# Optimization experiments

Measured on AMD Instinct MI355X. Metric: run time of the kernel, lower is better.

Reference implementation:

```python
import jax, jax.numpy as jnp
import numpy as np

B, T, F, H, OUT = 32, 2048, 64, 256, 64
EPS = 1e-3  # Keras LayerNormalization default epsilon


def _gru(x_seq, kernel, rkernel, bias, return_sequences):
    """Keras GRU (reset_after=True). x_seq: [B,T,Fin]; kernel [Fin,3H]; rkernel [H,3H]; bias [2,3H]."""
    h = x_seq.shape[-1]
    Hd = rkernel.shape[0]
    # precompute input projections for all timesteps (one big GEMM)
    xb = jnp.einsum('btf,fg->btg', x_seq, kernel) + bias[0]  # [B,T,3H]

    def step(h_prev, xt):
        inner = h_prev @ rkernel + bias[1]            # [B,3H]
        xz, xr, xh = jnp.split(xt, 3, axis=-1)
        rz, rr, rh = jnp.split(inner, 3, axis=-1)
        z = jax.nn.sigmoid(xz + rz)
        r = jax.nn.sigmoid(xr + rr)
        hh = jnp.tanh(xh + r * rh)
        h_new = z * h_prev + (1.0 - z) * hh
        return h_new, h_new

    h0 = jnp.zeros((x_seq.shape[0], Hd), dtype=x_seq.dtype)
    h_last, seq = jax.lax.scan(step, h0, jnp.swapaxes(xb, 0, 1))  # scan over T
    if return_sequences:
        return jnp.swapaxes(seq, 0, 1)  # [B,T,H]
    return h_last  # [B,H]


def setup_inputs() -> dict:
    key = jax.random.key(0)
    ks = jax.random.split(key, 10)
    s = 0.05
    return {
        'x': jax.random.normal(ks[0], (B, T, F), dtype=jnp.float32),
        'gamma': jnp.ones((F,), jnp.float32),
        'beta': jnp.zeros((F,), jnp.float32),
        'k1': jax.random.normal(ks[1], (F, 3 * H), jnp.float32) * s,
        'rk1': jax.random.normal(ks[2], (H, 3 * H), jnp.float32) * s,
        'b1': jnp.zeros((2, 3 * H), jnp.float32),
        'k2': jax.random.normal(ks[3], (H, 3 * H), jnp.float32) * s,
        'rk2': jax.random.normal(ks[4], (H, 3 * H), jnp.float32) * s,
        'b2': jnp.zeros((2, 3 * H), jnp.float32),
        'wd': jax.random.normal(ks[5], (H, OUT), jnp.float32) * s,
        'bd': jnp.zeros((OUT,), jnp.float32),
    }


def reference(x, gamma, beta, k1, rk1, b1, k2, rk2, b2, wd, bd):
    # LayerNorm over last (feature) axis
    mu = jnp.mean(x, axis=-1, keepdims=True)
    var = jnp.mean(jnp.square(x - mu), axis=-1, keepdims=True)
    xn = (x - mu) * jax.lax.rsqrt(var + EPS) * gamma + beta
    h1 = _gru(xn, k1, rk1, b1, return_sequences=True)   # [B,T,H]
    h2 = _gru(h1, k2, rk2, b2, return_sequences=False)  # [B,H]
    return h2 @ wd + bd  # [B,OUT]
```

## Files before the change

kernel.cpp:

```cpp
#include <hip/hip_runtime.h>

#define B_    32
#define T_    2048
#define F_    64
#define H_    256
#define OUT_  64
#define G3_   768
#define NWG1  16
#define NWG2  16
#define TOTAL_WG (NWG1 + NWG2)
#define WGT   512

#define PBLK   512
#define XN_BYTES (B_ * T_ * F_ * 2)
#define S1_OFF   XN_BYTES
#define S2_OFF   (S1_OFF + 4 * 16 * PBLK * 2)
#define FLAG_OFF (S2_OFF + 2 * 16 * PBLK * 2)
#define PROG_OFF (FLAG_OFF + 2048)

typedef _Float16 half8 __attribute__((ext_vector_type(8)));
typedef _Float16 half4 __attribute__((ext_vector_type(4)));
typedef float    f32x4 __attribute__((ext_vector_type(4)));
typedef unsigned long long u64;

#define LD_A(p)    __hip_atomic_load((p),  __ATOMIC_RELAXED, __HIP_MEMORY_SCOPE_AGENT)
#define ST_A(p, v) __hip_atomic_store((p), (v), __ATOMIC_RELAXED, __HIP_MEMORY_SCOPE_AGENT)

__device__ __forceinline__ float sigf(float x) {
    x = fminf(fmaxf(x, -30.f), 30.f);
    return 1.f / (1.f + __expf(-x));
}
__device__ __forceinline__ float tanhfast(float x) {
    x = fminf(fmaxf(x, -15.f), 15.f);
    float e = __expf(2.f * x);
    return (e - 1.f) / (e + 1.f);
}
__device__ __forceinline__ unsigned short f16b(float f) {
    union { _Float16 h; unsigned short u; } c; c.h = (_Float16)f; return c.u;
}
__device__ __forceinline__ u64 gather4(unsigned short u, int jl) {
    unsigned int p = (unsigned int)__shfl_xor((int)(unsigned int)u, 1);
    unsigned int lo32 = (jl & 1) ? ((p & 0xffffu) | ((unsigned int)u << 16))
                                 : ((unsigned int)u | (p << 16));
    unsigned int q = (unsigned int)__shfl_xor((int)lo32, 2);
    return (jl & 2) ? (((u64)lo32 << 32) | q)
                    : ((u64)lo32 | ((u64)q << 32));
}

__global__ void init_kernel(float* __restrict__ out, const float* __restrict__ bd,
                            _Float16* __restrict__ packs, unsigned int* __restrict__ flg) {
    int t = blockIdx.x * 256 + threadIdx.x;
    if (t < B_ * OUT_) out[t] = bd[t & (OUT_ - 1)];
    if (t < 1024) flg[t] = 0u;
    for (int p = t; p < 6 * 16 * PBLK; p += 4096) packs[p] = (_Float16)0.f;
}

__global__ __launch_bounds__(256) void ln_kernel(const float* __restrict__ x,
                                                 const float* __restrict__ gamma,
                                                 const float* __restrict__ beta,
                                                 _Float16* __restrict__ xn) {
    const int tid = threadIdx.x;
    const int r = tid >> 4, q = tid & 15;
    const size_t row = (size_t)blockIdx.x * 16 + r;
    const int b = (int)(row >> 11);
    const int t = (int)(row & 2047);
    const float4 v  = *(const float4*)(x + row * F_ + q * 4);
    const float4 g  = *(const float4*)(gamma + q * 4);
    const float4 be = *(const float4*)(beta + q * 4);
    float s = v.x + v.y + v.z + v.w;
    s += __shfl_xor(s, 1, 16); s += __shfl_xor(s, 2, 16);
    s += __shfl_xor(s, 4, 16); s += __shfl_xor(s, 8, 16);
    const float mu = s * (1.f / 64.f);
    const float dx = v.x - mu, dy = v.y - mu, dz = v.z - mu, dw = v.w - mu;
    float qq = dx * dx + dy * dy + dz * dz + dw * dw;
    qq += __shfl_xor(qq, 1, 16); qq += __shfl_xor(qq, 2, 16);
    qq += __shfl_xor(qq, 4, 16); qq += __shfl_xor(qq, 8, 16);
    const float rs = rsqrtf(qq * (1.f / 64.f) + 1e-3f);
    half4 o;
    o[0] = (_Float16)(dx * rs * g.x + be.x);
    o[1] = (_Float16)(dy * rs * g.y + be.y);
    o[2] = (_Float16)(dz * rs * g.z + be.z);
    o[3] = (_Float16)(dw * rs * g.w + be.w);
    *(half4*)(xn + ((size_t)t * B_ + b) * F_ + q * 4) = o;
}

__global__ __launch_bounds__(WGT) void gru_main(
    const _Float16* __restrict__ xn,
    const float* __restrict__ k1, const float* __restrict__ rk1,
    const float* __restrict__ b1, const float* __restrict__ k2,
    const float* __restrict__ rk2, const float* __restrict__ b2,
    const float* __restrict__ wd, float* __restrict__ out,
    _Float16* __restrict__ p1, _Float16* __restrict__ p2,
    unsigned int* __restrict__ flags, unsigned int* __restrict__ prog) {
    const int tid  = threadIdx.x;
    const int lane = tid & 63;
    const int wave = tid >> 6;
    const int mt   = wave & 1;
    const int nt   = wave >> 1;
    const int ln   = lane & 15;
    const int quad = lane >> 4;

    __shared__ _Float16 h1s[32][264];
    __shared__ _Float16 h2s[32][264];
    __shared__ float Cs[2][32][52];
    __shared__ float hs[32][16];

    const int  lc    = nt * 16 + ln;
    const bool valid = (lc < 48);
    const int  gate  = lc >> 4;
    const int  hidx  = lc & 15;
    const int  jl    = tid & 15;
    const int  bb    = tid >> 4;
    const int  m     = mt * 16 + ln;

    if (blockIdx.x < NWG1) {
        const int w    = blockIdx.x;
        const int gcol = valid ? (gate * H_ + w * 16 + hidx) : 0;
        half8 fk1[2], frk1[8];
#pragma unroll
        for (int ks = 0; ks < 2; ++ks) {
            half8 f;
#pragma unroll
            for (int j = 0; j < 8; ++j) {
                const float v = k1[(ks * 32 + quad * 8 + j) * G3_ + gcol];
                f[j] = valid ? (_Float16)v : (_Float16)0.f;
            }
            fk1[ks] = f;
        }
#pragma unroll
        for (int ks = 0; ks < 8; ++ks) {
            half8 f;
#pragma unroll
            for (int j = 0; j < 8; ++j) {
                const float v = rk1[(ks * 32 + quad * 8 + j) * G3_ + gcol];
                f[j] = valid ? (_Float16)v : (_Float16)0.f;
            }
            frk1[ks] = f;
        }
        const int gc = w * 16 + jl;
        const float bxz = b1[gc],       bxr = b1[H_ + gc],       bxh = b1[2 * H_ + gc];
        const float bhz = b1[G3_ + gc], bhr = b1[G3_ + H_ + gc], bhh = b1[G3_ + 2 * H_ + gc];
        float h1m = 0.f;

        const int w2  = tid >> 5;
        const int t32 = tid & 31;
        const unsigned* f1p = flags + w2 * 16;
        const unsigned* f2p = prog  + w2 * 16;

        for (int i = 0; i < T_; ++i) {
            f32x4 c0 = {0.f, 0.f, 0.f, 0.f};
            {
                half8 ax0 = *(const half8*)(xn + ((size_t)i * B_ + m) * F_ + quad * 8);
                half8 ax1 = *(const half8*)(xn + ((size_t)i * B_ + m) * F_ + 32 + quad * 8);
                c0 = __builtin_amdgcn_mfma_f32_16x16x32_f16(ax0, fk1[0], c0, 0, 0, 0);
                c0 = __builtin_amdgcn_mfma_f32_16x16x32_f16(ax1, fk1[1], c0, 0, 0, 0);
            }
            {
                const unsigned tgt1 = (unsigned)i;
                const unsigned tgt2 = (i >= 4) ? (unsigned)(i - 3) : 0u;
                while (LD_A(f1p) < tgt1 || LD_A(f2p) < tgt2)
                    __builtin_amdgcn_s_sleep(1);
                const u64* src = (const u64*)(p1 + (((unsigned)(i + 3) & 3u) * 16 + w2) * PBLK);
                u64 q0 = LD_A(src + t32);
                u64 q1 = LD_A(src + 32 + t32);
                u64 q2 = LD_A(src + 64 + t32);
                u64 q3 = LD_A(src + 96 + t32);
                const int b0 = t32 >> 2;
                const int c0f = w2 * 16 + (t32 & 3) * 4;
                *(u64*)(&h1s[b0][c0f])      = q0;
                *(u64*)(&h1s[b0 + 8][c0f])  = q1;
                *(u64*)(&h1s[b0 + 16][c0f]) = q2;
                *(u64*)(&h1s[b0 + 24][c0f]) = q3;
            }
            __syncthreads();

            f32x4 c1 = {0.f, 0.f, 0.f, 0.f};
#pragma unroll
            for (int ks = 0; ks < 8; ++ks) {
                half8 a1 = *(const half8*)(&h1s[m][ks * 32 + quad * 8]);
                c1 = __builtin_amdgcn_mfma_f32_16x16x32_f16(a1, frk1[ks], c1, 0, 0, 0);
            }
            if (valid) {
                const int r0 = mt * 16 + quad * 4;
#pragma unroll
                for (int rr = 0; rr < 4; ++rr) {
                    Cs[0][r0 + rr][lc] = c0[rr];
                    Cs[1][r0 + rr][lc] = c1[rr];
                }
            }
            __syncthreads();

            {
                const float xz = Cs[0][bb][jl]      + bxz;
                const float xr = Cs[0][bb][16 + jl] + bxr;
                const float xh = Cs[0][bb][32 + jl] + bxh;
                const float rz = Cs[1][bb][jl]      + bhz;
                const float rr = Cs[1][bb][16 + jl] + bhr;
                const float rh = Cs[1][bb][32 + jl] + bhh;
                const float z  = sigf(xz + rz);
                const float r  = sigf(xr + rr);
                const float hh = tanhfast(xh + r * rh);
                h1m = z * h1m + (1.f - z) * hh;
                const u64 v1 = gather4(f16b(h1m), jl);
                if ((jl & 3) == 0)
                    ST_A((u64*)(p1 + ((unsigned)(i & 3) * 16 + w) * PBLK + bb * 16 + jl), v1);
                asm volatile("s_waitcnt vmcnt(0)" ::: "memory");
            }
            __syncthreads();
            if (tid == 0) ST_A(&flags[w * 16], (unsigned)(i + 1));
        }
    } else {
        const int w    = blockIdx.x - NWG1;
        const int gcol = valid ? (gate * H_ + w * 16 + hidx) : 0;
        half8 fk2[8], frk2[8];
#pragma unroll
        for (int ks = 0; ks < 8; ++ks) {
            half8 f2, f3;
#pragma unroll
            for (int j = 0; j < 8; ++j) {
                const int k = ks * 32 + quad * 8 + j;
                const float v2 = k2 [k * G3_ + gcol];
                const float v3 = rk2[k * G3_ + gcol];
                f2[j] = valid ? (_Float16)v2 : (_Float16)0.f;
                f3[j] = valid ? (_Float16)v3 : (_Float16)0.f;
            }
            fk2[ks] = f2; frk2[ks] = f3;
        }
        const int gc = w * 16 + jl;
        const float bxz = b2[gc],       bxr = b2[H_ + gc],       bxh = b2[2 * H_ + gc];
        const float bhz = b2[G3_ + gc], bhr = b2[G3_ + H_ + gc], bhh = b2[G3_ + 2 * H_ + gc];
        float h2m = 0.f;

        const int pk  = tid >> 8;
        const int tt  = tid & 255;
        const int w2  = tt >> 4;
        const int l16 = tt & 15;
        const unsigned* fp = pk ? (flags + (16 + w2) * 16) : (flags + w2 * 16);

        for (int t = 0; t < T_; ++t) {
            {
                const unsigned tgt = pk ? (unsigned)t : (unsigned)(t + 1);
                while (LD_A(fp) < tgt) __builtin_amdgcn_s_sleep(1);
                const u64* src = pk
                    ? (const u64*)(p2 + (((unsigned)(t + 1) & 1u) * 16 + w2) * PBLK)
                    : (const u64*)(p1 + (((unsigned)t & 3u) * 16 + w2) * PBLK);
                u64 q[8];
#pragma unroll
                for (int k = 0; k < 8; ++k) q[k] = LD_A(src + k * 16 + l16);
                _Float16 (*dst)[264] = pk ? h2s : h1s;
                const int c0f = w2 * 16 + (l16 & 3) * 4;
                const int b0  = l16 >> 2;
#pragma unroll
                for (int k = 0; k < 8; ++k)
                    *(u64*)(&dst[b0 + k * 4][c0f]) = q[k];
            }
            __syncthreads();
            if (tid == 0) ST_A(&prog[w * 16], (unsigned)(t + 1));

            f32x4 c2 = {0.f, 0.f, 0.f, 0.f};
            f32x4 c3 = c2;
#pragma unroll
            for (int ks = 0; ks < 8; ++ks) {
                half8 a1 = *(const half8*)(&h1s[m][ks * 32 + quad * 8]);
                half8 a2 = *(const half8*)(&h2s[m][ks * 32 + quad * 8]);
                c2 = __builtin_amdgcn_mfma_f32_16x16x32_f16(a1, fk2[ks],  c2, 0, 0, 0);
                c3 = __builtin_amdgcn_mfma_f32_16x16x32_f16(a2, frk2[ks], c3, 0, 0, 0);
            }
            if (valid) {
                const int r0 = mt * 16 + quad * 4;
#pragma unroll
                for (int rr = 0; rr < 4; ++rr) {
                    Cs[0][r0 + rr][lc] = c2[rr];
                    Cs[1][r0 + rr][lc] = c3[rr];
                }
            }
            __syncthreads();

            {
                const float xz = Cs[0][bb][jl]      + bxz;
                const float xr = Cs[0][bb][16 + jl] + bxr;
                const float xh = Cs[0][bb][32 + jl] + bxh;
                const float rz = Cs[1][bb][jl]      + bhz;
                const float rr = Cs[1][bb][16 + jl] + bhr;
                const float rh = Cs[1][bb][32 + jl] + bhh;
                const float z  = sigf(xz + rz);
                const float r  = sigf(xr + rr);
                const float hh = tanhfast(xh + r * rh);
                h2m = z * h2m + (1.f - z) * hh;
                const u64 v2 = gather4(f16b(h2m), jl);
                if ((jl & 3) == 0)
                    ST_A((u64*)(p2 + ((unsigned)(t & 1) * 16 + w) * PBLK + bb * 16 + jl), v2);
                asm volatile("s_waitcnt vmcnt(0)" ::: "memory");
            }
            __syncthreads();
            if (tid == 0) ST_A(&flags[(16 + w) * 16], (unsigned)(t + 1));
        }

        hs[bb][jl] = h2m;
        __syncthreads();
        const int o  = tid & 63;
        const int bq = tid >> 6;
        for (int pass = 0; pass < 4; ++pass) {
            const int b = pass * 8 + bq;
            float acc = 0.f;
#pragma unroll
            for (int j = 0; j < 16; ++j) acc += hs[b][j] * wd[(w * 16 + j) * OUT_ + o];
            atomicAdd(&out[b * OUT_ + o], acc);
        }
    }
}

extern "C" void kernel_launch(void* const* d_in, const int* in_sizes, int n_in,
                              void* d_out, int out_size, void* d_ws, size_t ws_size,
                              hipStream_t stream) {
    const float* x     = (const float*)d_in[0];
    const float* gamma = (const float*)d_in[1];
    const float* beta  = (const float*)d_in[2];
    const float* k1    = (const float*)d_in[3];
    const float* rk1   = (const float*)d_in[4];
    const float* b1    = (const float*)d_in[5];
    const float* k2    = (const float*)d_in[6];
    const float* rk2   = (const float*)d_in[7];
    const float* b2    = (const float*)d_in[8];
    const float* wd    = (const float*)d_in[9];
    const float* bd    = (const float*)d_in[10];
    float* out = (float*)d_out;

    char* ws = (char*)d_ws;
    _Float16*     xn    = (_Float16*)ws;
    _Float16*     p1    = (_Float16*)(ws + S1_OFF);
    _Float16*     p2    = (_Float16*)(ws + S2_OFF);
    unsigned int* flags = (unsigned int*)(ws + FLAG_OFF);
    unsigned int* prog  = (unsigned int*)(ws + PROG_OFF);

    hipLaunchKernelGGL(init_kernel, dim3(16), dim3(256), 0, stream, out, bd, p1, flags);
    hipLaunchKernelGGL(ln_kernel, dim3(B_ * T_ / 16), dim3(256), 0, stream, x, gamma, beta, xn);

    void* args[] = {(void*)&xn, (void*)&k1, (void*)&rk1, (void*)&b1, (void*)&k2,
                    (void*)&rk2, (void*)&b2, (void*)&wd, (void*)&out,
                    (void*)&p1, (void*)&p2, (void*)&flags, (void*)&prog};
    hipLaunchCooperativeKernel((void*)gru_main, dim3(TOTAL_WG), dim3(WGT), args, 0, stream);
}
```

Baseline: 5.621 ms.

## Replace flag-based handoff with step-tagged hidden-state packets and deeper ring buffers

Each published fp16 hidden value now carries its timestep tag in the upper 16 bits, so consumers poll the data itself rather than a separate flag. This removes the vmcnt wait, the extra barrier and the flag store per step on the producer side. The ring buffers are deepened (16 slots for layer 1, 4 for layer 2) so the backpressure constraint is looser, and the input projection load is hoisted ahead of the wait. The cost is doubled packet bytes and repeated reloading of whole packets while spinning, plus a 16-bit tag that wraps at 65536 steps.

```diff
diff --git a/kernel.cpp b/kernel.cpp
--- a/kernel.cpp
+++ b/kernel.cpp
@@ -11,18 +11,22 @@
 #define TOTAL_WG (NWG1 + NWG2)
 #define WGT   512
 
-#define PBLK   512
+#define D1    16
+#define D2    4
+#define BLK_W 512
+
 #define XN_BYTES (B_ * T_ * F_ * 2)
-#define S1_OFF   XN_BYTES
-#define S2_OFF   (S1_OFF + 4 * 16 * PBLK * 2)
-#define FLAG_OFF (S2_OFF + 2 * 16 * PBLK * 2)
-#define PROG_OFF (FLAG_OFF + 2048)
+#define P1_OFF   XN_BYTES
+#define P2_OFF   (P1_OFF + D1 * 16 * BLK_W * 4)
+#define PROG_OFF (P2_OFF + D2 * 16 * BLK_W * 4)
 
 typedef _Float16 half8 __attribute__((ext_vector_type(8)));
 typedef _Float16 half4 __attribute__((ext_vector_type(4)));
 typedef float    f32x4 __attribute__((ext_vector_type(4)));
 typedef unsigned long long u64;
 
+#define TAGMASK 0xFFFF0000FFFF0000ull
+
 #define LD_A(p)    __hip_atomic_load((p),  __ATOMIC_RELAXED, __HIP_MEMORY_SCOPE_AGENT)
 #define ST_A(p, v) __hip_atomic_store((p), (v), __ATOMIC_RELAXED, __HIP_MEMORY_SCOPE_AGENT)
 
@@ -38,21 +42,13 @@
 __device__ __forceinline__ unsigned short f16b(float f) {
     union { _Float16 h; unsigned short u; } c; c.h = (_Float16)f; return c.u;
 }
-__device__ __forceinline__ u64 gather4(unsigned short u, int jl) {
-    unsigned int p = (unsigned int)__shfl_xor((int)(unsigned int)u, 1);
-    unsigned int lo32 = (jl & 1) ? ((p & 0xffffu) | ((unsigned int)u << 16))
-                                 : ((unsigned int)u | (p << 16));
-    unsigned int q = (unsigned int)__shfl_xor((int)lo32, 2);
-    return (jl & 2) ? (((u64)lo32 << 32) | q)
-                    : ((u64)lo32 | ((u64)q << 32));
-}
 
 __global__ void init_kernel(float* __restrict__ out, const float* __restrict__ bd,
-                            _Float16* __restrict__ packs, unsigned int* __restrict__ flg) {
+                            unsigned int* __restrict__ packs, unsigned int* __restrict__ prog) {
     int t = blockIdx.x * 256 + threadIdx.x;
     if (t < B_ * OUT_) out[t] = bd[t & (OUT_ - 1)];
-    if (t < 1024) flg[t] = 0u;
-    for (int p = t; p < 6 * 16 * PBLK; p += 4096) packs[p] = (_Float16)0.f;
+    if (t < 1024) prog[t] = 0u;
+    for (int p = t; p < (D1 + D2) * 16 * BLK_W; p += 4096) packs[p] = 0u;
 }
 
 __global__ __launch_bounds__(256) void ln_kernel(const float* __restrict__ x,
@@ -90,8 +86,8 @@
     const float* __restrict__ b1, const float* __restrict__ k2,
     const float* __restrict__ rk2, const float* __restrict__ b2,
     const float* __restrict__ wd, float* __restrict__ out,
-    _Float16* __restrict__ p1, _Float16* __restrict__ p2,
-    unsigned int* __restrict__ flags, unsigned int* __restrict__ prog) {
+    unsigned int* __restrict__ p1u, unsigned int* __restrict__ p2u,
+    unsigned int* __restrict__ prog) {
     const int tid  = threadIdx.x;
     const int lane = tid & 63;
     const int wave = tid >> 6;
@@ -113,6 +109,12 @@
     const int  bb    = tid >> 4;
     const int  m     = mt * 16 + ln;
 
+    for (int p = tid; p < 32 * 264; p += WGT) {
+        ((_Float16*)h1s)[p] = (_Float16)0.f;
+        ((_Float16*)h2s)[p] = (_Float16)0.f;
+    }
+    __syncthreads();
+
     if (blockIdx.x < NWG1) {
         const int w    = blockIdx.x;
         const int gcol = valid ? (gate * H_ + w * 16 + hidx) : 0;
@@ -144,36 +146,46 @@
 
         const int w2  = tid >> 5;
         const int t32 = tid & 31;
-        const unsigned* f1p = flags + w2 * 16;
-        const unsigned* f2p = prog  + w2 * 16;
+        const unsigned* bpp = prog + w2 * 16;
 
         for (int i = 0; i < T_; ++i) {
+            const _Float16* xr = xn + ((size_t)i * B_ + m) * F_ + quad * 8;
+            const half8 ax0 = *(const half8*)(xr);
+            const half8 ax1 = *(const half8*)(xr + 32);
+
+            if (i > 0) {
+                const unsigned tag = (unsigned)i;
+                const u64 tp = ((u64)tag << 48) | ((u64)tag << 16);
+                const u64* src = (const u64*)(p1u + (((unsigned)(i - 1) & (D1 - 1)) * 16 + w2) * BLK_W);
+                const unsigned bp = (i >= 13) ? (unsigned)(i - 12) : 0u;
+                u64 q[8];
+                for (;;) {
+                    bool ok = (LD_A(bpp) >= bp);
+#pragma unroll
+                    for (int k = 0; k < 4; ++k) {
+                        q[2 * k]     = LD_A(src + 64 * k + 2 * t32);
+                        q[2 * k + 1] = LD_A(src + 64 * k + 2 * t32 + 1);
+                    }
+#pragma unroll
+                    for (int k = 0; k < 8; ++k) ok &= ((q[k] & TAGMASK) == tp);
+                    if (ok) break;
+                    __builtin_amdgcn_s_sleep(1);
+                }
+                const int c0f = w2 * 16 + (t32 & 3) * 4;
+                const int br  = t32 >> 2;
+#pragma unroll
+                for (int k = 0; k < 4; ++k) {
+                    const u64 q0 = q[2 * k], q1 = q[2 * k + 1];
+                    const u64 h4 = (q0 & 0xFFFFull) | ((q0 >> 16) & 0xFFFF0000ull)
+                                 | ((q1 & 0xFFFFull) << 32) | ((q1 & 0xFFFF00000000ull) << 16);
+                    *(u64*)(&h1s[br + 8 * k][c0f]) = h4;
+                }
+            }
+            __syncthreads();
+
             f32x4 c0 = {0.f, 0.f, 0.f, 0.f};
-            {
-                half8 ax0 = *(const half8*)(xn + ((size_t)i * B_ + m) * F_ + quad * 8);
-                half8 ax1 = *(const half8*)(xn + ((size_t)i * B_ + m) * F_ + 32 + quad * 8);
-                c0 = __builtin_amdgcn_mfma_f32_16x16x32_f16(ax0, fk1[0], c0, 0, 0, 0);
-                c0 = __builtin_amdgcn_mfma_f32_16x16x32_f16(ax1, fk1[1], c0, 0, 0, 0);
-            }
-            {
-                const unsigned tgt1 = (unsigned)i;
-                const unsigned tgt2 = (i >= 4) ? (unsigned)(i - 3) : 0u;
-                while (LD_A(f1p) < tgt1 || LD_A(f2p) < tgt2)
-                    __builtin_amdgcn_s_sleep(1);
-                const u64* src = (const u64*)(p1 + (((unsigned)(i + 3) & 3u) * 16 + w2) * PBLK);
-                u64 q0 = LD_A(src + t32);
-                u64 q1 = LD_A(src + 32 + t32);
-                u64 q2 = LD_A(src + 64 + t32);
-                u64 q3 = LD_A(src + 96 + t32);
-                const int b0 = t32 >> 2;
-                const int c0f = w2 * 16 + (t32 & 3) * 4;
-                *(u64*)(&h1s[b0][c0f])      = q0;
-                *(u64*)(&h1s[b0 + 8][c0f])  = q1;
-                *(u64*)(&h1s[b0 + 16][c0f]) = q2;
-                *(u64*)(&h1s[b0 + 24][c0f]) = q3;
-            }
-            __syncthreads();
-
+            c0 = __builtin_amdgcn_mfma_f32_16x16x32_f16(ax0, fk1[0], c0, 0, 0, 0);
+            c0 = __builtin_amdgcn_mfma_f32_16x16x32_f16(ax1, fk1[1], c0, 0, 0, 0);
             f32x4 c1 = {0.f, 0.f, 0.f, 0.f};
 #pragma unroll
             for (int ks = 0; ks < 8; ++ks) {
@@ -192,22 +204,22 @@
 
             {
                 const float xz = Cs[0][bb][jl]      + bxz;
-                const float xr = Cs[0][bb][16 + jl] + bxr;
+                const float xr2 = Cs[0][bb][16 + jl] + bxr;
                 const float xh = Cs[0][bb][32 + jl] + bxh;
                 const float rz = Cs[1][bb][jl]      + bhz;
                 const float rr = Cs[1][bb][16 + jl] + bhr;
                 const float rh = Cs[1][bb][32 + jl] + bhh;
                 const float z  = sigf(xz + rz);
-                const float r  = sigf(xr + rr);
+                const float r  = sigf(xr2 + rr);
                 const float hh = tanhfast(xh + r * rh);
                 h1m = z * h1m + (1.f - z) * hh;
-                const u64 v1 = gather4(f16b(h1m), jl);
-                if ((jl & 3) == 0)
-                    ST_A((u64*)(p1 + ((unsigned)(i & 3) * 16 + w) * PBLK + bb * 16 + jl), v1);
-                asm volatile("s_waitcnt vmcnt(0)" ::: "memory");
-            }
-            __syncthreads();
-            if (tid == 0) ST_A(&flags[w * 16], (unsigned)(i + 1));
+                const unsigned wv = (unsigned)f16b(h1m) | ((unsigned)(i + 1) << 16);
+                const unsigned pv = (unsigned)__shfl_xor((int)wv, 1);
+                if ((jl & 1) == 0) {
+                    const u64 v1 = (u64)wv | ((u64)pv << 32);
+                    ST_A((u64*)(p1u + (((unsigned)i & (D1 - 1)) * 16 + w) * BLK_W + bb * 16 + jl), v1);
+                }
+            }
         }
     } else {
         const int w    = blockIdx.x - NWG1;
@@ -235,24 +247,37 @@
         const int tt  = tid & 255;
         const int w2  = tt >> 4;
         const int l16 = tt & 15;
-        const unsigned* fp = pk ? (flags + (16 + w2) * 16) : (flags + w2 * 16);
 
         for (int t = 0; t < T_; ++t) {
-            {
-                const unsigned tgt = pk ? (unsigned)t : (unsigned)(t + 1);
-                while (LD_A(fp) < tgt) __builtin_amdgcn_s_sleep(1);
+            if (pk == 0 || t > 0) {
+                const unsigned tag = pk ? (unsigned)t : (unsigned)(t + 1);
+                const u64 tp = ((u64)tag << 48) | ((u64)tag << 16);
                 const u64* src = pk
-                    ? (const u64*)(p2 + (((unsigned)(t + 1) & 1u) * 16 + w2) * PBLK)
-                    : (const u64*)(p1 + (((unsigned)t & 3u) * 16 + w2) * PBLK);
-                u64 q[8];
-#pragma unroll
-                for (int k = 0; k < 8; ++k) q[k] = LD_A(src + k * 16 + l16);
+                    ? (const u64*)(p2u + (((unsigned)(t - 1) & (D2 - 1)) * 16 + w2) * BLK_W)
+                    : (const u64*)(p1u + (((unsigned)t & (D1 - 1)) * 16 + w2) * BLK_W);
+                u64 q[16];
+                for (;;) {
+                    bool ok = true;
+#pragma unroll
+                    for (int k = 0; k < 8; ++k) {
+                        q[2 * k]     = LD_A(src + 32 * k + 2 * l16);
+                        q[2 * k + 1] = LD_A(src + 32 * k + 2 * l16 + 1);
+                    }
+#pragma unroll
+                    for (int k = 0; k < 16; ++k) ok &= ((q[k] & TAGMASK) == tp);
+                    if (ok) break;
+                    __builtin_amdgcn_s_sleep(1);
+                }
                 _Float16 (*dst)[264] = pk ? h2s : h1s;
                 const int c0f = w2 * 16 + (l16 & 3) * 4;
-                const int b0  = l16 >> 2;
-#pragma unroll
-                for (int k = 0; k < 8; ++k)
-                    *(u64*)(&dst[b0 + k * 4][c0f]) = q[k];
+                const int br  = l16 >> 2;
+#pragma unroll
+                for (int k = 0; k < 8; ++k) {
+                    const u64 q0 = q[2 * k], q1 = q[2 * k + 1];
+                    const u64 h4 = (q0 & 0xFFFFull) | ((q0 >> 16) & 0xFFFF0000ull)
+                                 | ((q1 & 0xFFFFull) << 32) | ((q1 & 0xFFFF00000000ull) << 16);
+                    *(u64*)(&dst[br + 4 * k][c0f]) = h4;
+                }
             }
             __syncthreads();
             if (tid == 0) ST_A(&prog[w * 16], (unsigned)(t + 1));
@@ -278,22 +303,22 @@
 
             {
                 const float xz = Cs[0][bb][jl]      + bxz;
-                const float xr = Cs[0][bb][16 + jl] + bxr;
+                const float xr2 = Cs[0][bb][16 + jl] + bxr;
                 const float xh = Cs[0][bb][32 + jl] + bxh;
                 const float rz = Cs[1][bb][jl]      + bhz;
                 const float rr = Cs[1][bb][16 + jl] + bhr;
                 const float rh = Cs[1][bb][32 + jl] + bhh;
                 const float z  = sigf(xz + rz);
-                const float r  = sigf(xr + rr);
+                const float r  = sigf(xr2 + rr);
                 const float hh = tanhfast(xh + r * rh);
                 h2m = z * h2m + (1.f - z) * hh;
-                const u64 v2 = gather4(f16b(h2m), jl);
-                if ((jl & 3) == 0)
-                    ST_A((u64*)(p2 + ((unsigned)(t & 1) * 16 + w) * PBLK + bb * 16 + jl), v2);
-                asm volatile("s_waitcnt vmcnt(0)" ::: "memory");
-            }
-            __syncthreads();
-            if (tid == 0) ST_A(&flags[(16 + w) * 16], (unsigned)(t + 1));
+                const unsigned wv = (unsigned)f16b(h2m) | ((unsigned)(t + 1) << 16);
+                const unsigned pv = (unsigned)__shfl_xor((int)wv, 1);
+                if ((jl & 1) == 0) {
+                    const u64 v2 = (u64)wv | ((u64)pv << 32);
+                    ST_A((u64*)(p2u + (((unsigned)t & (D2 - 1)) * 16 + w) * BLK_W + bb * 16 + jl), v2);
+                }
+            }
         }
 
         hs[bb][jl] = h2m;
@@ -327,17 +352,16 @@
     float* out = (float*)d_out;
 
     char* ws = (char*)d_ws;
-    _Float16*     xn    = (_Float16*)ws;
-    _Float16*     p1    = (_Float16*)(ws + S1_OFF);
-    _Float16*     p2    = (_Float16*)(ws + S2_OFF);
-    unsigned int* flags = (unsigned int*)(ws + FLAG_OFF);
-    unsigned int* prog  = (unsigned int*)(ws + PROG_OFF);
-
-    hipLaunchKernelGGL(init_kernel, dim3(16), dim3(256), 0, stream, out, bd, p1, flags);
+    _Float16*     xn   = (_Float16*)ws;
+    unsigned int* p1u  = (unsigned int*)(ws + P1_OFF);
+    unsigned int* p2u  = (unsigned int*)(ws + P2_OFF);
+    unsigned int* prog = (unsigned int*)(ws + PROG_OFF);
+
+    hipLaunchKernelGGL(init_kernel, dim3(16), dim3(256), 0, stream, out, bd, p1u, prog);
     hipLaunchKernelGGL(ln_kernel, dim3(B_ * T_ / 16), dim3(256), 0, stream, x, gamma, beta, xn);
 
     void* args[] = {(void*)&xn, (void*)&k1, (void*)&rk1, (void*)&b1, (void*)&k2,
                     (void*)&rk2, (void*)&b2, (void*)&wd, (void*)&out,
-                    (void*)&p1, (void*)&p2, (void*)&flags, (void*)&prog};
+                    (void*)&p1u, (void*)&p2u, (void*)&prog};
     hipLaunchCooperativeKernel((void*)gru_main, dim3(TOTAL_WG), dim3(WGT), args, 0, stream);
 }
```

Measured after the change: 6.272 ms. +11.6%, slower.
